# Optimization experiments

Measured on AMD Instinct MI355X. Metric: run time of the kernel, lower is better.

Reference implementation:

```python
import jax, jax.numpy as jnp
import numpy as np

D_MODEL = 1024
NUM_HEADS = 16
D_K = D_MODEL // NUM_HEADS
B, S = 4, 2048


def setup_inputs() -> dict:
    key = jax.random.key(0)
    ks = jax.random.split(key, 12)
    scale = 1.0 / np.sqrt(D_MODEL)
    inp = {
        "query": jax.random.normal(ks[0], (B, S, D_MODEL), jnp.float32),
        "key": jax.random.normal(ks[1], (B, S, D_MODEL), jnp.float32),
        "value": jax.random.normal(ks[2], (B, S, D_MODEL), jnp.float32),
        # causal mask, broadcastable over (batch, heads)
        "mask": jnp.tril(jnp.ones((S, S), jnp.int32))[None, None, :, :],
        "Wq": jax.random.normal(ks[3], (D_MODEL, D_MODEL), jnp.float32) * scale,
        "bq": jnp.zeros((D_MODEL,), jnp.float32),
        "Wk": jax.random.normal(ks[4], (D_MODEL, D_MODEL), jnp.float32) * scale,
        "bk": jnp.zeros((D_MODEL,), jnp.float32),
        "Wv": jax.random.normal(ks[5], (D_MODEL, D_MODEL), jnp.float32) * scale,
        "bv": jnp.zeros((D_MODEL,), jnp.float32),
        "Wo": jax.random.normal(ks[6], (D_MODEL, D_MODEL), jnp.float32) * scale,
        "bo": jnp.zeros((D_MODEL,), jnp.float32),
    }
    return inp


def reference(query, key, value, mask, Wq, bq, Wk, bk, Wv, bv, Wo, bo):
    b = query.shape[0]
    # projections (torch Linear: x @ W.T + b)
    Q = query @ Wq.T + bq
    K = key @ Wk.T + bk
    V = value @ Wv.T + bv
    # [B, S, D] -> [B, H, S, d_k]
    def split_heads(x):
        return x.reshape(b, -1, NUM_HEADS, D_K).transpose(0, 2, 1, 3)
    Q, K, V = split_heads(Q), split_heads(K), split_heads(V)
    # scaled dot-product attention, full score matrix as in original
    scores = jnp.einsum("bhqd,bhkd->bhqk", Q, K) / jnp.sqrt(jnp.float32(D_K))
    scores = jnp.where(mask == 0, jnp.float32(-jnp.inf), scores)
    attn = jax.nn.softmax(scores, axis=-1)  # dropout p=0.0 -> identity
    x = jnp.einsum("bhqk,bhkd->bhqd", attn, V)
    # [B, H, S, d_k] -> [B, S, D]
    x = x.transpose(0, 2, 1, 3).reshape(b, -1, D_MODEL)
    return x @ Wo.T + bo
```

## Files before the change

### kernel.cpp

```cpp
#include <hip/hip_runtime.h>
#include <hip/hip_bf16.h>
#include <stdint.h>

#define D_MODEL 1024
#define NUM_HEADS 16
#define DK 64
#define BATCH 4
#define SEQ 2048
#define MTOT (BATCH * SEQ)

typedef unsigned short u16;
typedef unsigned int u32;
typedef __bf16 bf16x8 __attribute__((ext_vector_type(8)));
typedef float f32x4 __attribute__((ext_vector_type(4)));
typedef short s16x4 __attribute__((ext_vector_type(4)));
typedef int   i32x4 __attribute__((ext_vector_type(4)));
typedef int   i32x2 __attribute__((ext_vector_type(2)));
typedef uint  u32x2 __attribute__((ext_vector_type(2)));

__device__ __forceinline__ f32x4 mfma16(s16x4 a, s16x4 b, f32x4 c) {
  return __builtin_amdgcn_mfma_f32_16x16x16bf16_1k(a, b, c, 0, 0, 0);
}

__device__ __forceinline__ u16 f2bf(float f) {
  union { float f; unsigned u; } c; c.f = f;
  unsigned u = c.u + 0x7fffu + ((c.u >> 16) & 1u);
  return (u16)(u >> 16);
}
__device__ __forceinline__ u32 pack_bf2(float f0, float f1) {
  return __builtin_amdgcn_perm(__float_as_uint(f1), __float_as_uint(f0), 0x07060302u);
}
__device__ __forceinline__ s16x4 cast_s16x4(u32 lo, u32 hi) {
  u32x2 t = {lo, hi};
  return (s16x4)t;
}

__device__ __forceinline__ void async16(void* g, void* lds) {
  __builtin_amdgcn_global_load_lds(
      (__attribute__((address_space(1))) void*)g,
      (__attribute__((address_space(3))) void*)lds,
      16, 0, 0);
}

struct CvtArgs {
  const float* s[7];
  u16* d[7];
  int n[7];
};
__global__ __launch_bounds__(256)
void cvt_multi(CvtArgs a) {
  const int which = blockIdx.y;
  const int n = a.n[which];
  const int i = (blockIdx.x * 256 + threadIdx.x) * 8;
  if (i >= n) return;
  const float* s = a.s[which];
  u16* d = a.d[which];
  const float4 x = *(const float4*)(s + i);
  const float4 y = *(const float4*)(s + i + 4);
  *(ushort4*)(d + i)     = make_ushort4(f2bf(x.x), f2bf(x.y), f2bf(x.z), f2bf(x.w));
  *(ushort4*)(d + i + 4) = make_ushort4(f2bf(y.x), f2bf(y.y), f2bf(y.z), f2bf(y.w));
}

template <bool VT_OUT, bool F32_OUT>
__global__ __launch_bounds__(256, 2)
void gemm_bt_bias(const u16* __restrict__ A, const u16* __restrict__ W,
                  const float* __restrict__ bias, void* __restrict__ Cv,
                  float oscale)
{
  __shared__ u16 As[128 * 32];
  __shared__ u16 Bs[128 * 32];
  const int t = threadIdx.x;
  const int w = t >> 6, l = t & 63;
  const int quad = l >> 4, lane16 = l & 15;
  const int m0 = blockIdx.x * 128;
  const int n0 = blockIdx.y * 128;
  const int wm = (w >> 1) * 64, wn = (w & 1) * 64;

  const int srow = t >> 2;
  const int scol = (t & 3) * 8;
  const u16* Ag = A + (long)(m0 + srow) * D_MODEL + scol;
  const u16* Wg = W + (long)(n0 + srow) * D_MODEL + scol;
  u16* As_w = As + w * 512;
  u16* Bs_w = Bs + w * 512;

  f32x4 acc[4][4] = {};

  for (int k0 = 0; k0 < D_MODEL; k0 += 32) {
    __syncthreads();
    async16((void*)(Ag + k0), As_w);
    async16((void*)(Ag + 64 * D_MODEL + k0), As_w + 2048);
    async16((void*)(Wg + k0), Bs_w);
    async16((void*)(Wg + 64 * D_MODEL + k0), Bs_w + 2048);
    __syncthreads();

    bf16x8 af[4], bfr[4];
#pragma unroll
    for (int i = 0; i < 4; ++i)
      af[i] = *(const bf16x8*)&As[(wm + i * 16 + lane16) * 32 + quad * 8];
#pragma unroll
    for (int i = 0; i < 4; ++i)
      bfr[i] = *(const bf16x8*)&Bs[(wn + i * 16 + lane16) * 32 + quad * 8];
#pragma unroll
    for (int i = 0; i < 4; ++i)
#pragma unroll
      for (int jn = 0; jn < 4; ++jn)
        acc[i][jn] = __builtin_amdgcn_mfma_f32_16x16x32_bf16(af[i], bfr[jn], acc[i][jn], 0, 0, 0);
  }

  if constexpr (VT_OUT) {
    __shared__ u16 T[128 * 132];
#pragma unroll
    for (int jn = 0; jn < 4; ++jn) {
      const int col = wn + jn * 16 + lane16;
      const float bb = bias[n0 + col];
#pragma unroll
      for (int i = 0; i < 4; ++i) {
        const int rbase = wm + i * 16 + quad * 4;
#pragma unroll
        for (int r = 0; r < 4; ++r)
          T[col * 132 + rbase + r] = f2bf((acc[i][jn][r] + bb) * oscale);
      }
    }
    __syncthreads();
    const int bq = m0 >> 11, sbase = m0 & 2047;
    const int a = t & 31;
    const int keystart = ((a >> 3) * 32) + (((a & 7) >> 1) * 4) + ((a & 1) * 16);
    u16* orow = (u16*)Cv + ((long)bq * 1024 + n0) * SEQ + sbase + 4 * a;
#pragma unroll
    for (int pass = 0; pass < 16; ++pass) {
      const int dkl = (t >> 5) + 8 * pass;
      *(u32x2*)(orow + (long)dkl * SEQ) = *(const u32x2*)&T[dkl * 132 + keystart];
    }
  } else {
#pragma unroll
    for (int jn = 0; jn < 4; ++jn) {
      const int col = n0 + wn + jn * 16 + lane16;
      const float bb = bias[col];
#pragma unroll
      for (int i = 0; i < 4; ++i) {
        const int rbase = m0 + wm + i * 16 + quad * 4;
#pragma unroll
        for (int r = 0; r < 4; ++r) {
          const float v = (acc[i][jn][r] + bb) * oscale;
          if (F32_OUT) ((float*)Cv)[(long)(rbase + r) * D_MODEL + col] = v;
          else         ((u16*)Cv)[(long)(rbase + r) * D_MODEL + col] = f2bf(v);
        }
      }
    }
  }
}

__global__ __launch_bounds__(256, 3)
void attn_causal(const u16* __restrict__ Q, const u16* __restrict__ K,
                 const u16* __restrict__ VtX, u16* __restrict__ O)
{
  __shared__ __align__(16) u16 Kb[2][32][72];
  __shared__ __align__(16) u16 Vb[2][64][40];
  const int t = threadIdx.x;
  const int w = t >> 6, l = t & 63;
  const int quad = l >> 4, lane16 = l & 15;

  const int lin = blockIdx.x;
  const int xcd = lin & 7;
  const int j = lin >> 3;
  const int bh = xcd * 8 + (j & 7);
  const int g = 15 - (j >> 3);
  const int b = bh >> 4, h = bh & 15;
  const int sw = 4 * g + w;
  const int cmax = 4 * g + 3;
  const int qbase = sw * 32;

  const long qkbase = (long)b * SEQ * D_MODEL + h * DK;

  bf16x8 qf[2][2];
#pragma unroll
  for (int qi = 0; qi < 2; ++qi)
#pragma unroll
    for (int ks = 0; ks < 2; ++ks)
      qf[qi][ks] = *(const bf16x8*)&Q[qkbase +
          (long)(qbase + qi * 16 + lane16) * D_MODEL + ks * 32 + quad * 8];

  const int krow = t >> 3, kc = t & 7;
  const char* Kgt = (const char*)(K + qkbase) + (long)krow * (D_MODEL * 2) + kc * 16;
  u16* KbD0 = &Kb[0][krow][kc * 8];
  u16* KbD1 = &Kb[1][krow][kc * 8];
  const int vrow = t >> 2, vc = t & 3;
  const char* Vgt = (const char*)(VtX + ((long)b * 1024 + h * 64) * SEQ) +
                    (long)vrow * (SEQ * 2) + vc * 16;
  u16* VbD0 = &Vb[0][vrow][vc * 8];
  u16* VbD1 = &Vb[1][vrow][vc * 8];

  f32x4 oacc[4][2] = {};
  float lsum[2] = {0.f, 0.f};

  auto body = [&](const u16 (*Kbuf)[72], const u16 (*Vbuf)[40], bool diag) {
    bf16x8 kf[2][2];
#pragma unroll
    for (int kt = 0; kt < 2; ++kt)
#pragma unroll
      for (int ks = 0; ks < 2; ++ks)
        kf[kt][ks] = *(const bf16x8*)&Kbuf[kt * 16 + lane16][ks * 32 + quad * 8];
    i32x4 vfd[4];
#pragma unroll
    for (int d = 0; d < 4; ++d)
      vfd[d] = *(const i32x4*)&Vbuf[d * 16 + lane16][quad * 8];

    f32x4 st[2][2] = {};
#pragma unroll
    for (int kt = 0; kt < 2; ++kt)
#pragma unroll
      for (int qi = 0; qi < 2; ++qi)
#pragma unroll
        for (int ks = 0; ks < 2; ++ks)
          st[kt][qi] = __builtin_amdgcn_mfma_f32_16x16x32_bf16(kf[kt][ks], qf[qi][ks], st[kt][qi], 0, 0, 0);

    u32 pb[2][2][2];
#pragma unroll
    for (int kt = 0; kt < 2; ++kt)
#pragma unroll
      for (int qi = 0; qi < 2; ++qi) {
        float pv[4];
#pragma unroll
        for (int r = 0; r < 4; ++r) {
          float p = __builtin_amdgcn_exp2f(st[kt][qi][r]);
          if (diag && (kt * 16 + quad * 4 + r > qi * 16 + lane16)) p = 0.f;
          pv[r] = p;
        }
        lsum[qi] += (pv[0] + pv[1]) + (pv[2] + pv[3]);
        pb[kt][qi][0] = pack_bf2(pv[0], pv[1]);
        pb[kt][qi][1] = pack_bf2(pv[2], pv[3]);
      }

#pragma unroll
    for (int d = 0; d < 4; ++d) {
      const s16x4 va0 = cast_s16x4((u32)vfd[d].x, (u32)vfd[d].y);
      const s16x4 va1 = cast_s16x4((u32)vfd[d].z, (u32)vfd[d].w);
#pragma unroll
      for (int qi = 0; qi < 2; ++qi) {
        const s16x4 pb0 = cast_s16x4(pb[0][qi][0], pb[0][qi][1]);
        const s16x4 pb1 = cast_s16x4(pb[1][qi][0], pb[1][qi][1]);
        oacc[d][qi] = mfma16(va0, pb0, oacc[d][qi]);
        oacc[d][qi] = mfma16(va1, pb1, oacc[d][qi]);
      }
    }
  };

  {
    i32x4 a0 = *(const i32x4*)(Kgt);
    i32x4 a1 = *(const i32x4*)(Vgt);
    *(i32x4*)KbD0 = a0;
    *(i32x4*)VbD0 = a1;
  }
  i32x4 gKA = *(const i32x4*)(Kgt + 65536);
  i32x4 gVA = *(const i32x4*)(Vgt + 64);
  i32x4 gKB = *(const i32x4*)(Kgt + 2 * 65536);
  i32x4 gVB = *(const i32x4*)(Vgt + 2 * 64);
  __syncthreads();

  for (int c = 0; c <= cmax; c += 2) {
    *(i32x4*)KbD1 = gKA;
    *(i32x4*)VbD1 = gVA;
    if (c + 3 <= cmax) {
      gKA = *(const i32x4*)(Kgt + (long)(c + 3) * 65536);
      gVA = *(const i32x4*)(Vgt + (long)(c + 3) * 64);
    }
    if (c <= sw) body(Kb[0], Vb[0], c == sw);
    __syncthreads();
    if (c + 2 <= cmax) {
      *(i32x4*)KbD0 = gKB;
      *(i32x4*)VbD0 = gVB;
      if (c + 4 <= cmax) {
        gKB = *(const i32x4*)(Kgt + (long)(c + 4) * 65536);
        gVB = *(const i32x4*)(Vgt + (long)(c + 4) * 64);
      }
    }
    if (c + 1 <= sw) body(Kb[1], Vb[1], (c + 1) == sw);
    __syncthreads();
  }

  float linv[2];
#pragma unroll
  for (int qi = 0; qi < 2; ++qi) {
    float v = lsum[qi];
    v += __shfl_xor(v, 16);
    v += __shfl_xor(v, 32);
    linv[qi] = 1.f / v;
  }

#pragma unroll
  for (int qi = 0; qi < 2; ++qi) {
    const long row = (long)b * SEQ + qbase + qi * 16 + lane16;
#pragma unroll
    for (int d = 0; d < 4; ++d) {
      const u32 p0 = ((u32)f2bf(oacc[d][qi][0] * linv[qi])) |
                     ((u32)f2bf(oacc[d][qi][1] * linv[qi]) << 16);
      const u32 p1 = ((u32)f2bf(oacc[d][qi][2] * linv[qi])) |
                     ((u32)f2bf(oacc[d][qi][3] * linv[qi]) << 16);
      u32x2 pk = {p0, p1};
      *(u32x2*)&O[row * D_MODEL + h * 64 + d * 16 + quad * 4] = pk;
    }
  }
}

extern "C" void kernel_launch(void* const* d_in, const int* in_sizes, int n_in,
                              void* d_out, int out_size, void* d_ws, size_t ws_size,
                              hipStream_t stream) {
  const float* q  = (const float*)d_in[0];
  const float* k  = (const float*)d_in[1];
  const float* v  = (const float*)d_in[2];
  const float* Wq = (const float*)d_in[4];
  const float* bq = (const float*)d_in[5];
  const float* Wk = (const float*)d_in[6];
  const float* bk = (const float*)d_in[7];
  const float* Wv = (const float*)d_in[8];
  const float* bv = (const float*)d_in[9];
  const float* Wo = (const float*)d_in[10];
  const float* bo = (const float*)d_in[11];
  float* out = (float*)d_out;

  const size_t NT = (size_t)MTOT * D_MODEL;
  const size_t NW = (size_t)D_MODEL * D_MODEL;

  u16* w0  = (u16*)d_ws;
  u16* qb  = w0;
  u16* kb  = w0 + NT;
  u16* vb  = w0 + 2 * NT;
  u16* Wqb = w0 + 3 * NT;
  u16* Wkb = Wqb + NW;
  u16* Wvb = Wqb + 2 * NW;
  u16* Wob = Wqb + 3 * NW;
  u16* Qp  = (u16*)d_out;
  u16* Kp  = (u16*)d_out + NT;
  u16* Vpt = qb;
  u16* Xp  = kb;

  const dim3 blk(256);

  CvtArgs ca;
  ca.s[0] = q;  ca.d[0] = qb;  ca.n[0] = (int)NT;
  ca.s[1] = k;  ca.d[1] = kb;  ca.n[1] = (int)NT;
  ca.s[2] = v;  ca.d[2] = vb;  ca.n[2] = (int)NT;
  ca.s[3] = Wq; ca.d[3] = Wqb; ca.n[3] = (int)NW;
  ca.s[4] = Wk; ca.d[4] = Wkb; ca.n[4] = (int)NW;
  ca.s[5] = Wv; ca.d[5] = Wvb; ca.n[5] = (int)NW;
  ca.s[6] = Wo; ca.d[6] = Wob; ca.n[6] = (int)NW;
  cvt_multi<<<dim3(4096, 7), blk, 0, stream>>>(ca);

  const float SC = 0.125f * 1.4426950408889634f;
  const dim3 ggrid(MTOT / 128, D_MODEL / 128);
  gemm_bt_bias<false, false><<<ggrid, blk, 0, stream>>>(qb, Wqb, bq, Qp, SC);
  gemm_bt_bias<false, false><<<ggrid, blk, 0, stream>>>(kb, Wkb, bk, Kp, 1.f);
  gemm_bt_bias<true,  false><<<ggrid, blk, 0, stream>>>(vb, Wvb, bv, Vpt, 1.f);

  const dim3 agrid(1024);
  attn_causal<<<agrid, blk, 0, stream>>>(Qp, Kp, Vpt, Xp);

  gemm_bt_bias<false, true><<<ggrid, blk, 0, stream>>>(Xp, Wob, bo, out, 1.f);
}
```

Baseline: 316.3 us.

## Double-buffer GEMM, batch QKV projections, swizzle attention LDS, add MFMA priority

The GEMM now double-buffers its LDS tiles, so the next k-slice is loaded asynchronously while the current one is computed. The three Q/K/V projection GEMMs are merged into a single launch using a z-dimension batch struct with a runtime output mode in place of template flags. The attention kernel drops its padded LDS rows in favour of XOR-swizzled layouts to avoid bank conflicts, and wraps the MFMA sections in s_setprio. The risks are runtime mode branches that are no longer compile-time, a larger LDS footprint per GEMM block, and changed occupancy.

Result: no change. 316.1 us (-0.1%).

```diff
diff --git a/kernel.cpp b/kernel.cpp
--- a/kernel.cpp
+++ b/kernel.cpp
@@ -40,6 +40,9 @@
       (__attribute__((address_space(1))) void*)g,
       (__attribute__((address_space(3))) void*)lds,
       16, 0, 0);
+}
+__device__ __forceinline__ void vm_drain() {
+  asm volatile("s_waitcnt vmcnt(0)" ::: "memory");
 }
 
 struct CvtArgs {
@@ -61,14 +64,27 @@
   *(ushort4*)(d + i + 4) = make_ushort4(f2bf(y.x), f2bf(y.y), f2bf(y.z), f2bf(y.w));
 }
 
-template <bool VT_OUT, bool F32_OUT>
+struct GBatch {
+  const u16* A[3]; const u16* W[3]; const float* bias[3];
+  void* C[3]; float osc[3]; int mode[3];
+};
 __global__ __launch_bounds__(256, 2)
-void gemm_bt_bias(const u16* __restrict__ A, const u16* __restrict__ W,
-                  const float* __restrict__ bias, void* __restrict__ Cv,
-                  float oscale)
+void gemm_bt_bias(GBatch ga)
 {
-  __shared__ u16 As[128 * 32];
-  __shared__ u16 Bs[128 * 32];
+  __shared__ __align__(16) u16 smem[16896];
+  u16* As0 = smem;
+  u16* Bs0 = smem + 4096;
+  u16* As1 = smem + 8192;
+  u16* Bs1 = smem + 12288;
+
+  const int z = blockIdx.z;
+  const u16* __restrict__ A = ga.A[z];
+  const u16* __restrict__ W = ga.W[z];
+  const float* __restrict__ bias = ga.bias[z];
+  void* __restrict__ Cv = ga.C[z];
+  const float oscale = ga.osc[z];
+  const int mode = ga.mode[z];
+
   const int t = threadIdx.x;
   const int w = t >> 6, l = t & 63;
   const int quad = l >> 4, lane16 = l & 15;
@@ -80,35 +96,47 @@
   const int scol = (t & 3) * 8;
   const u16* Ag = A + (long)(m0 + srow) * D_MODEL + scol;
   const u16* Wg = W + (long)(n0 + srow) * D_MODEL + scol;
-  u16* As_w = As + w * 512;
-  u16* Bs_w = Bs + w * 512;
 
   f32x4 acc[4][4] = {};
 
-  for (int k0 = 0; k0 < D_MODEL; k0 += 32) {
-    __syncthreads();
-    async16((void*)(Ag + k0), As_w);
-    async16((void*)(Ag + 64 * D_MODEL + k0), As_w + 2048);
-    async16((void*)(Wg + k0), Bs_w);
-    async16((void*)(Wg + 64 * D_MODEL + k0), Bs_w + 2048);
-    __syncthreads();
-
+  auto stage = [&](u16* As_, u16* Bs_, int k0) {
+    async16((void*)(Ag + k0), As_ + w * 512);
+    async16((void*)(Ag + 64 * D_MODEL + k0), As_ + w * 512 + 2048);
+    async16((void*)(Wg + k0), Bs_ + w * 512);
+    async16((void*)(Wg + 64 * D_MODEL + k0), Bs_ + w * 512 + 2048);
+  };
+  auto compute = [&](const u16* As_, const u16* Bs_) {
     bf16x8 af[4], bfr[4];
 #pragma unroll
     for (int i = 0; i < 4; ++i)
-      af[i] = *(const bf16x8*)&As[(wm + i * 16 + lane16) * 32 + quad * 8];
+      af[i] = *(const bf16x8*)&As_[(wm + i * 16 + lane16) * 32 + quad * 8];
 #pragma unroll
     for (int i = 0; i < 4; ++i)
-      bfr[i] = *(const bf16x8*)&Bs[(wn + i * 16 + lane16) * 32 + quad * 8];
+      bfr[i] = *(const bf16x8*)&Bs_[(wn + i * 16 + lane16) * 32 + quad * 8];
 #pragma unroll
     for (int i = 0; i < 4; ++i)
 #pragma unroll
       for (int jn = 0; jn < 4; ++jn)
         acc[i][jn] = __builtin_amdgcn_mfma_f32_16x16x32_bf16(af[i], bfr[jn], acc[i][jn], 0, 0, 0);
-  }
-
-  if constexpr (VT_OUT) {
-    __shared__ u16 T[128 * 132];
+  };
+
+  stage(As0, Bs0, 0);
+  vm_drain();
+  __syncthreads();
+#pragma unroll 1
+  for (int k0 = 0; k0 < D_MODEL; k0 += 64) {
+    stage(As1, Bs1, k0 + 32);
+    compute(As0, Bs0);
+    vm_drain();
+    __syncthreads();
+    if (k0 + 64 < D_MODEL) stage(As0, Bs0, k0 + 64);
+    compute(As1, Bs1);
+    vm_drain();
+    __syncthreads();
+  }
+
+  if (mode == 1) {
+    u16* T = smem;
 #pragma unroll
     for (int jn = 0; jn < 4; ++jn) {
       const int col = wn + jn * 16 + lane16;
@@ -142,8 +170,8 @@
 #pragma unroll
         for (int r = 0; r < 4; ++r) {
           const float v = (acc[i][jn][r] + bb) * oscale;
-          if (F32_OUT) ((float*)Cv)[(long)(rbase + r) * D_MODEL + col] = v;
-          else         ((u16*)Cv)[(long)(rbase + r) * D_MODEL + col] = f2bf(v);
+          if (mode == 2) ((float*)Cv)[(long)(rbase + r) * D_MODEL + col] = v;
+          else           ((u16*)Cv)[(long)(rbase + r) * D_MODEL + col] = f2bf(v);
         }
       }
     }
@@ -154,8 +182,8 @@
 void attn_causal(const u16* __restrict__ Q, const u16* __restrict__ K,
                  const u16* __restrict__ VtX, u16* __restrict__ O)
 {
-  __shared__ __align__(16) u16 Kb[2][32][72];
-  __shared__ __align__(16) u16 Vb[2][64][40];
+  __shared__ __align__(16) u16 Kb[2][32][64];
+  __shared__ __align__(16) u16 Vb[2][64][32];
   const int t = threadIdx.x;
   const int w = t >> 6, l = t & 63;
   const int quad = l >> 4, lane16 = l & 15;
@@ -182,30 +210,33 @@
 
   const int krow = t >> 3, kc = t & 7;
   const char* Kgt = (const char*)(K + qkbase) + (long)krow * (D_MODEL * 2) + kc * 16;
-  u16* KbD0 = &Kb[0][krow][kc * 8];
-  u16* KbD1 = &Kb[1][krow][kc * 8];
+  u16* KbD0 = &Kb[0][krow][(kc ^ (krow & 7)) * 8];
+  u16* KbD1 = &Kb[1][krow][(kc ^ (krow & 7)) * 8];
   const int vrow = t >> 2, vc = t & 3;
   const char* Vgt = (const char*)(VtX + ((long)b * 1024 + h * 64) * SEQ) +
                     (long)vrow * (SEQ * 2) + vc * 16;
-  u16* VbD0 = &Vb[0][vrow][vc * 8];
-  u16* VbD1 = &Vb[1][vrow][vc * 8];
+  u16* VbD0 = &Vb[0][vrow][(vc ^ (vrow & 3)) * 8];
+  u16* VbD1 = &Vb[1][vrow][(vc ^ (vrow & 3)) * 8];
 
   f32x4 oacc[4][2] = {};
   float lsum[2] = {0.f, 0.f};
 
-  auto body = [&](const u16 (*Kbuf)[72], const u16 (*Vbuf)[40], bool diag) {
+  auto body = [&](const u16 (*Kbuf)[64], const u16 (*Vbuf)[32], bool diag) {
     bf16x8 kf[2][2];
 #pragma unroll
     for (int kt = 0; kt < 2; ++kt)
 #pragma unroll
       for (int ks = 0; ks < 2; ++ks)
-        kf[kt][ks] = *(const bf16x8*)&Kbuf[kt * 16 + lane16][ks * 32 + quad * 8];
+        kf[kt][ks] = *(const bf16x8*)
+            &Kbuf[kt * 16 + lane16][(((ks * 4 + quad) ^ (lane16 & 7)) * 8)];
     i32x4 vfd[4];
 #pragma unroll
     for (int d = 0; d < 4; ++d)
-      vfd[d] = *(const i32x4*)&Vbuf[d * 16 + lane16][quad * 8];
+      vfd[d] = *(const i32x4*)
+          &Vbuf[d * 16 + lane16][((quad ^ (lane16 & 3)) * 8)];
 
     f32x4 st[2][2] = {};
+    __builtin_amdgcn_s_setprio(1);
 #pragma unroll
     for (int kt = 0; kt < 2; ++kt)
 #pragma unroll
@@ -213,6 +244,7 @@
 #pragma unroll
         for (int ks = 0; ks < 2; ++ks)
           st[kt][qi] = __builtin_amdgcn_mfma_f32_16x16x32_bf16(kf[kt][ks], qf[qi][ks], st[kt][qi], 0, 0, 0);
+    __builtin_amdgcn_s_setprio(0);
 
     u32 pb[2][2][2];
 #pragma unroll
@@ -231,6 +263,7 @@
         pb[kt][qi][1] = pack_bf2(pv[2], pv[3]);
       }
 
+    __builtin_amdgcn_s_setprio(1);
 #pragma unroll
     for (int d = 0; d < 4; ++d) {
       const s16x4 va0 = cast_s16x4((u32)vfd[d].x, (u32)vfd[d].y);
@@ -243,6 +276,7 @@
         oacc[d][qi] = mfma16(va1, pb1, oacc[d][qi]);
       }
     }
+    __builtin_amdgcn_s_setprio(0);
   };
 
   {
@@ -347,13 +381,20 @@
   cvt_multi<<<dim3(4096, 7), blk, 0, stream>>>(ca);
 
   const float SC = 0.125f * 1.4426950408889634f;
-  const dim3 ggrid(MTOT / 128, D_MODEL / 128);
-  gemm_bt_bias<false, false><<<ggrid, blk, 0, stream>>>(qb, Wqb, bq, Qp, SC);
-  gemm_bt_bias<false, false><<<ggrid, blk, 0, stream>>>(kb, Wkb, bk, Kp, 1.f);
-  gemm_bt_bias<true,  false><<<ggrid, blk, 0, stream>>>(vb, Wvb, bv, Vpt, 1.f);
+
+  GBatch g1;
+  g1.A[0] = qb; g1.W[0] = Wqb; g1.bias[0] = bq; g1.C[0] = Qp;  g1.osc[0] = SC;  g1.mode[0] = 0;
+  g1.A[1] = kb; g1.W[1] = Wkb; g1.bias[1] = bk; g1.C[1] = Kp;  g1.osc[1] = 1.f; g1.mode[1] = 0;
+  g1.A[2] = vb; g1.W[2] = Wvb; g1.bias[2] = bv; g1.C[2] = Vpt; g1.osc[2] = 1.f; g1.mode[2] = 1;
+  gemm_bt_bias<<<dim3(MTOT / 128, D_MODEL / 128, 3), blk, 0, stream>>>(g1);
 
   const dim3 agrid(1024);
   attn_causal<<<agrid, blk, 0, stream>>>(Qp, Kp, Vpt, Xp);
 
-  gemm_bt_bias<false, true><<<ggrid, blk, 0, stream>>>(Xp, Wob, bo, out, 1.f);
-}
+  GBatch g2;
+  for (int i = 0; i < 3; ++i) {
+    g2.A[i] = Xp; g2.W[i] = Wob; g2.bias[i] = bo; g2.C[i] = out;
+    g2.osc[i] = 1.f; g2.mode[i] = 2;
+  }
+  gemm_bt_bias<<<dim3(MTOT / 128, D_MODEL / 128, 1), blk, 0, stream>>>(g2);
+}
```
